# Performance work log

Measured on AMD Instinct MI355X. Metric: run time of the kernel, lower is better.

## Reference

```python
import jax, jax.numpy as jnp
import numpy as np

DIM = 64
SQRT_DIM = np.sqrt(DIM).astype(np.float32)
NEG_INF = -1e9


def setup_inputs() -> dict:
    key = jax.random.key(0)
    kq, kk, kv, km = jax.random.split(key, 4)
    B, Q, K, D = 32, 1024, 1024, DIM
    query = jax.random.normal(kq, (B, Q, D), dtype=jnp.float32)
    k = jax.random.normal(kk, (B, K, D), dtype=jnp.float32)
    value = jax.random.normal(kv, (B, K, D), dtype=jnp.float32)
    mask = jax.random.randint(km, (B, Q, K), 0, 2).astype(jnp.bool_)
    return {"query": query, "key": k, "value": value, "mask": mask}


def reference(query, key, value, mask):
    # score: [B, Q, K]
    score = jnp.einsum('bqd,bkd->bqk', query, key) / SQRT_DIM
    score = jnp.where(mask, NEG_INF, score)
    attn = jax.nn.softmax(score, axis=-1)
    context = jnp.einsum('bqk,bkd->bqd', attn, value)
    return (context, attn)
```

## Files before the change

### kernel.cpp

```cpp
#include <hip/hip_runtime.h>

constexpr int BATCH = 32;
constexpr int QLEN  = 1024;
constexpr int KLEN  = 1024;
constexpr int DIM   = 64;
constexpr int TQ    = 16;

typedef float    f32x4 __attribute__((ext_vector_type(4)));
typedef int      i32x4 __attribute__((ext_vector_type(4)));
typedef _Float16 f16x8 __attribute__((ext_vector_type(8)));
typedef _Float16 f16x4 __attribute__((ext_vector_type(4)));
typedef unsigned long long u64;
typedef unsigned int u32;

__device__ __forceinline__ f16x8 cvt_h8(f32x4 a, f32x4 b) {
  f16x8 h;
  h[0] = (_Float16)a[0]; h[1] = (_Float16)a[1]; h[2] = (_Float16)a[2]; h[3] = (_Float16)a[3];
  h[4] = (_Float16)b[0]; h[5] = (_Float16)b[1]; h[6] = (_Float16)b[2]; h[7] = (_Float16)b[3];
  return h;
}

constexpr int TK = 128;
__global__ __launch_bounds__(256)
void vtkh_kernel(const float* __restrict__ V, const float* __restrict__ Kg,
                 _Float16* __restrict__ Vt, _Float16* __restrict__ Kh) {
  __shared__ _Float16 lt[DIM][TK + 8];
  const int b = blockIdx.y, k0 = blockIdx.x * TK;
  const int t = threadIdx.x;
  const int d4 = (t & 15) * 4;
  #pragma unroll
  for (int p = 0; p < TK / 16; ++p) {
    const int kl = (t >> 4) + p * 16;
    const f32x4 v = *(const f32x4*)(V + ((size_t)(b * KLEN + k0 + kl)) * DIM + d4);
    #pragma unroll
    for (int j = 0; j < 4; ++j) lt[d4 + j][kl] = (_Float16)v[j];
  }
  #pragma unroll
  for (int p = 0; p < 8; ++p) {
    const int idx = t + p * 256;
    const int kl = idx >> 4, dd = (idx & 15) * 4;
    const f32x4 v = *(const f32x4*)(Kg + ((size_t)(b * KLEN + k0 + kl)) * DIM + dd);
    f16x4 h = { (_Float16)v[0], (_Float16)v[1], (_Float16)v[2], (_Float16)v[3] };
    *(f16x4*)(Kh + ((size_t)(b * KLEN + k0 + kl)) * DIM + dd) = h;
  }
  __syncthreads();
  const int d = t >> 2;
  #pragma unroll
  for (int j2 = 0; j2 < TK / 32; ++j2) {
    const int seg = (t & 3) + j2 * 4;
    *(f16x8*)(Vt + (size_t)b * DIM * KLEN + (size_t)d * KLEN + k0 + seg * 8) =
        *(const f16x8*)(&lt[d][seg * 8]);
  }
}

__global__ __launch_bounds__(256, 4)
void sdpa_kernel(const float* __restrict__ Qg, const _Float16* __restrict__ Kh,
                 const _Float16* __restrict__ Vt, const int* __restrict__ Mg,
                 float* __restrict__ Ctx, float* __restrict__ Attn)
{
  __shared__ float rs[4][16];
  __shared__ float cx[4][16][65];

  const int tid  = threadIdx.x;
  const int w    = tid >> 6;
  const int l    = tid & 63;
  const int n16  = l & 15;
  const int quad = l >> 4;

  const int lin  = blockIdx.x;
  const int nlin = (lin & 7) * (BATCH * (QLEN / TQ) / 8) + (lin >> 3);
  const int b    = nlin >> 6;
  const int q0   = (nlin & 63) * TQ;

  const float qscl = 0.125f * 1.44269504f;
  const float* qb = Qg + ((size_t)(b * QLEN + q0 + n16)) * DIM + quad * 8;
  f32x4 qa0 = *(const f32x4*)(qb),      qa1 = *(const f32x4*)(qb + 4);
  f32x4 qa2 = *(const f32x4*)(qb + 32), qa3 = *(const f32x4*)(qb + 36);
  #pragma unroll
  for (int i = 0; i < 4; ++i) { qa0[i] *= qscl; qa1[i] *= qscl; qa2[i] *= qscl; qa3[i] *= qscl; }
  const f16x8 aq0 = cvt_h8(qa0, qa1);
  const f16x8 aq1 = cvt_h8(qa2, qa3);

  const _Float16* kb = Kh + (size_t)b * KLEN * DIM + quad * 8;
  const int* mrow = Mg + ((size_t)(b * QLEN + q0 + n16)) * KLEN + w * 256 + quad * 4;

  f32x4 rsum4 = {0.f, 0.f, 0.f, 0.f};
  f16x4 ec[16];
  #pragma unroll
  for (int tt = 0; tt < 16; ++tt) {
    const i32x4 mv = *(const i32x4*)(mrow + tt * 16);
    const _Float16* kp = kb + (size_t)((w * 16 + tt) * 16 + n16) * DIM;
    const f16x8 ak0 = *(const f16x8*)(kp);
    const f16x8 ak1 = *(const f16x8*)(kp + 32);
    f32x4 acc = {0.f, 0.f, 0.f, 0.f};
    acc = __builtin_amdgcn_mfma_f32_16x16x32_f16(ak0, aq0, acc, 0, 0, 0);
    acc = __builtin_amdgcn_mfma_f32_16x16x32_f16(ak1, aq1, acc, 0, 0, 0);
    f32x4 e;
    #pragma unroll
    for (int i = 0; i < 4; ++i) {
      e[i] = mv[i] ? 0.f : __builtin_amdgcn_exp2f(acc[i]);
      rsum4[i] += e[i];
    }
    ec[tt] = f16x4{ (_Float16)e[0], (_Float16)e[1], (_Float16)e[2], (_Float16)e[3] };
  }
  float rsum = (rsum4[0] + rsum4[1]) + (rsum4[2] + rsum4[3]);
  rsum += __shfl_xor(rsum, 16, 64);
  rsum += __shfl_xor(rsum, 32, 64);
  if (quad == 0) rs[w][n16] = rsum;
  __syncthreads();
  const float inv =
      __builtin_amdgcn_rcpf(rs[0][n16] + rs[1][n16] + rs[2][n16] + rs[3][n16]);

  float* arow = Attn + ((size_t)(b * QLEN + q0 + n16)) * KLEN + w * 256;
  const _Float16* vtb = Vt + (size_t)b * DIM * KLEN;
  f32x4 cacc[4] = { {0.f,0.f,0.f,0.f}, {0.f,0.f,0.f,0.f}, {0.f,0.f,0.f,0.f}, {0.f,0.f,0.f,0.f} };
  #pragma unroll
  for (int m = 0; m < 8; ++m) {
    uint2 pw[2];
    #pragma unroll
    for (int h = 0; h < 2; ++h) {
      const int tt = m * 2 + h;
      f32x4 ev;
      #pragma unroll
      for (int i = 0; i < 4; ++i) ev[i] = (float)ec[tt][i] * inv;
      *(f32x4*)(arow + tt * 16 + quad * 4) = ev;
      f16x4 ph = { (_Float16)ev[0], (_Float16)ev[1], (_Float16)ev[2], (_Float16)ev[3] };
      __builtin_memcpy(&pw[h], &ph, 8);
    }
    const int s0 = n16 + ((quad & 1) << 5);
    const u32 x0a = (u32)__shfl((int)pw[0].x, s0, 64);
    const u32 y0a = (u32)__shfl((int)pw[0].y, s0, 64);
    const u32 x1a = (u32)__shfl((int)pw[1].x, s0, 64);
    const u32 y1a = (u32)__shfl((int)pw[1].y, s0, 64);
    const u32 x0b = (u32)__shfl((int)pw[0].x, s0 + 16, 64);
    const u32 y0b = (u32)__shfl((int)pw[0].y, s0 + 16, 64);
    const u32 x1b = (u32)__shfl((int)pw[1].x, s0 + 16, 64);
    const u32 y1b = (u32)__shfl((int)pw[1].y, s0 + 16, 64);
    const bool hs = (quad & 2) != 0;
    const u32 dd[4] = { hs ? x1a : x0a, hs ? y1a : y0a,
                        hs ? x1b : x0b, hs ? y1b : y0b };
    f16x8 pa; __builtin_memcpy(&pa, dd, 16);
    const int K0 = w * 256 + m * 32;
    #pragma unroll
    for (int dt = 0; dt < 4; ++dt) {
      const f16x8 bv = *(const f16x8*)(vtb + (size_t)(dt * 16 + n16) * KLEN + K0 + quad * 8);
      cacc[dt] = __builtin_amdgcn_mfma_f32_16x16x32_f16(pa, bv, cacc[dt], 0, 0, 0);
    }
  }

  #pragma unroll
  for (int dt = 0; dt < 4; ++dt)
    #pragma unroll
    for (int i = 0; i < 4; ++i)
      cx[w][quad * 4 + i][dt * 16 + n16] = cacc[dt][i];
  __syncthreads();
  #pragma unroll
  for (int rr = 0; rr < 4; ++rr) {
    const int row = w * 4 + rr;
    const float v = (cx[0][row][l] + cx[1][row][l]) + (cx[2][row][l] + cx[3][row][l]);
    Ctx[((size_t)(b * QLEN + q0 + row)) * DIM + l] = v;
  }
}

extern "C" void kernel_launch(void* const* d_in, const int* in_sizes, int n_in,
                              void* d_out, int out_size, void* d_ws, size_t ws_size,
                              hipStream_t stream) {
  const float* Qg = (const float*)d_in[0];
  const float* Kg = (const float*)d_in[1];
  const float* Vg = (const float*)d_in[2];
  const int*   Mg = (const int*)d_in[3];
  float* Ctx  = (float*)d_out;
  float* Attn = (float*)d_out + (size_t)BATCH * QLEN * DIM;
  _Float16* Vt = (_Float16*)d_ws;
  _Float16* Kh = (_Float16*)((char*)d_ws + (size_t)BATCH * DIM * KLEN * 2);

  dim3 tgrid(KLEN / TK, BATCH);
  vtkh_kernel<<<tgrid, 256, 0, stream>>>(Vg, Kg, Vt, Kh);

  sdpa_kernel<<<2048, 256, 0, stream>>>(Qg, Kh, Vt, Mg, Ctx, Attn);
}
```

Baseline: 321.4 us.

## Stage probabilities in LDS, coalesce attn stores, split PV by head dim

Normalized probabilities are written as fp16 into a swizzled shared-memory tile covering the full 16x1024 block. The attn output is then written row-contiguously with nontemporal float4 stores. The PV matmul is re-partitioned so each wave owns 16 output dims over the full K range. This removes the lane shuffles and the cross-wave reduction of context partials, at the cost of 32KB of LDS per block, which may reduce occupancy.

```diff
diff --git a/kernel.cpp b/kernel.cpp
--- a/kernel.cpp
+++ b/kernel.cpp
@@ -59,13 +59,14 @@
                  float* __restrict__ Ctx, float* __restrict__ Attn)
 {
   __shared__ float rs[4][16];
-  __shared__ float cx[4][16][65];
+  __shared__ __attribute__((aligned(16))) _Float16 sp[TQ * 1024];
 
   const int tid  = threadIdx.x;
   const int w    = tid >> 6;
   const int l    = tid & 63;
   const int n16  = l & 15;
   const int quad = l >> 4;
+  char* const spb = (char*)sp;
 
   const int lin  = blockIdx.x;
   const int nlin = (lin & 7) * (BATCH * (QLEN / TQ) / 8) + (lin >> 3);
@@ -111,55 +112,44 @@
   const float inv =
       __builtin_amdgcn_rcpf(rs[0][n16] + rs[1][n16] + rs[2][n16] + rs[3][n16]);
 
-  float* arow = Attn + ((size_t)(b * QLEN + q0 + n16)) * KLEN + w * 256;
-  const _Float16* vtb = Vt + (size_t)b * DIM * KLEN;
-  f32x4 cacc[4] = { {0.f,0.f,0.f,0.f}, {0.f,0.f,0.f,0.f}, {0.f,0.f,0.f,0.f}, {0.f,0.f,0.f,0.f} };
   #pragma unroll
-  for (int m = 0; m < 8; ++m) {
-    uint2 pw[2];
+  for (int tt = 0; tt < 16; ++tt) {
+    f32x4 ev;
     #pragma unroll
-    for (int h = 0; h < 2; ++h) {
-      const int tt = m * 2 + h;
-      f32x4 ev;
-      #pragma unroll
-      for (int i = 0; i < 4; ++i) ev[i] = (float)ec[tt][i] * inv;
-      *(f32x4*)(arow + tt * 16 + quad * 4) = ev;
-      f16x4 ph = { (_Float16)ev[0], (_Float16)ev[1], (_Float16)ev[2], (_Float16)ev[3] };
-      __builtin_memcpy(&pw[h], &ph, 8);
-    }
-    const int s0 = n16 + ((quad & 1) << 5);
-    const u32 x0a = (u32)__shfl((int)pw[0].x, s0, 64);
-    const u32 y0a = (u32)__shfl((int)pw[0].y, s0, 64);
-    const u32 x1a = (u32)__shfl((int)pw[1].x, s0, 64);
-    const u32 y1a = (u32)__shfl((int)pw[1].y, s0, 64);
-    const u32 x0b = (u32)__shfl((int)pw[0].x, s0 + 16, 64);
-    const u32 y0b = (u32)__shfl((int)pw[0].y, s0 + 16, 64);
-    const u32 x1b = (u32)__shfl((int)pw[1].x, s0 + 16, 64);
-    const u32 y1b = (u32)__shfl((int)pw[1].y, s0 + 16, 64);
-    const bool hs = (quad & 2) != 0;
-    const u32 dd[4] = { hs ? x1a : x0a, hs ? y1a : y0a,
-                        hs ? x1b : x0b, hs ? y1b : y0b };
-    f16x8 pa; __builtin_memcpy(&pa, dd, 16);
-    const int K0 = w * 256 + m * 32;
+    for (int i = 0; i < 4; ++i) ev[i] = (float)ec[tt][i] * inv;
+    f16x4 ph = { (_Float16)ev[0], (_Float16)ev[1], (_Float16)ev[2], (_Float16)ev[3] };
+    const int g = w * 64 + tt * 4 + quad;
+    *(f16x4*)(spb + (n16 << 11) + ((g * 8) ^ ((n16 & 7) << 4))) = ph;
+  }
+  __syncthreads();
+
+  #pragma unroll
+  for (int rr = 0; rr < 4; ++rr) {
+    const int row = w * 4 + rr;
+    float* arow = Attn + ((size_t)(b * QLEN + q0 + row)) * KLEN;
     #pragma unroll
-    for (int dt = 0; dt < 4; ++dt) {
-      const f16x8 bv = *(const f16x8*)(vtb + (size_t)(dt * 16 + n16) * KLEN + K0 + quad * 8);
-      cacc[dt] = __builtin_amdgcn_mfma_f32_16x16x32_f16(pa, bv, cacc[dt], 0, 0, 0);
+    for (int j = 0; j < 4; ++j) {
+      const int g = j * 64 + l;
+      const f16x4 hv = *(const f16x4*)(spb + (row << 11) + ((g * 8) ^ ((row & 7) << 4)));
+      f32x4 ov = { (float)hv[0], (float)hv[1], (float)hv[2], (float)hv[3] };
+      __builtin_nontemporal_store(ov, (f32x4*)(arow + j * 256 + l * 4));
     }
   }
 
-  #pragma unroll
-  for (int dt = 0; dt < 4; ++dt)
-    #pragma unroll
-    for (int i = 0; i < 4; ++i)
-      cx[w][quad * 4 + i][dt * 16 + n16] = cacc[dt][i];
-  __syncthreads();
-  #pragma unroll
-  for (int rr = 0; rr < 4; ++rr) {
-    const int row = w * 4 + rr;
-    const float v = (cx[0][row][l] + cx[1][row][l]) + (cx[2][row][l] + cx[3][row][l]);
-    Ctx[((size_t)(b * QLEN + q0 + row)) * DIM + l] = v;
+  const _Float16* vtb = Vt + ((size_t)(b * DIM + w * 16 + n16)) * KLEN;
+  f32x4 c0 = {0.f, 0.f, 0.f, 0.f}, c1 = {0.f, 0.f, 0.f, 0.f};
+  #pragma unroll 8
+  for (int m = 0; m < 32; m += 2) {
+    const int ga = m * 8 + quad * 2;
+    const f16x8 pa0 = *(const f16x8*)(spb + (n16 << 11) + ((ga * 8) ^ ((n16 & 7) << 4)));
+    const f16x8 pa1 = *(const f16x8*)(spb + (n16 << 11) + (((ga + 8) * 8) ^ ((n16 & 7) << 4)));
+    const f16x8 bv0 = *(const f16x8*)(vtb + m * 32 + quad * 8);
+    const f16x8 bv1 = *(const f16x8*)(vtb + (m + 1) * 32 + quad * 8);
+    c0 = __builtin_amdgcn_mfma_f32_16x16x32_f16(bv0, pa0, c0, 0, 0, 0);
+    c1 = __builtin_amdgcn_mfma_f32_16x16x32_f16(bv1, pa1, c1, 0, 0, 0);
   }
+  f32x4 cv = { c0[0] + c1[0], c0[1] + c1[1], c0[2] + c1[2], c0[3] + c1[3] };
+  *(f32x4*)(Ctx + ((size_t)(b * QLEN + q0 + n16)) * DIM + w * 16 + quad * 4) = cv;
 }
 
 extern "C" void kernel_launch(void* const* d_in, const int* in_sizes, int n_in,
```

Result: faster. 306.1 us (-4.8%).
